# Performance work log

Measured on AMD Instinct MI355X. Metric: run time of the kernel, lower is better.

Reference implementation:

```python
import jax
jax.config.update("jax_enable_x64", True)
import jax.numpy as jnp
import numpy as np

B = 1_000_000

def _generators():
    # 8 sl(3) basis elements, each scaled by its (unit) weight, float64.
    e = np.zeros((8, 3, 3), dtype=np.float64)
    e[0, 0, 2] = 1.0                      # x translation
    e[1, 1, 2] = 1.0                      # y translation
    e[2, 0, 1] = -1.0; e[2, 1, 0] = 1.0   # rotation
    e[3, 0, 0] = 1.0; e[3, 1, 1] = 1.0; e[3, 2, 2] = -2.0  # scale
    e[4, 0, 0] = 1.0; e[4, 1, 1] = -1.0   # stretch
    e[5, 0, 1] = 1.0; e[5, 1, 0] = 1.0    # shear
    e[6, 2, 0] = 1.0                      # x keystone
    e[7, 2, 1] = 1.0                      # y keystone
    weights = np.ones((8,), dtype=np.float64)  # all weight kwargs default to 1.0
    return jnp.asarray(e * weights[:, None, None])

_GEN = _generators()

def setup_inputs() -> dict:
    key = jax.random.key(0)
    lie_vectors = jax.random.normal(key, (B, 8), dtype=jnp.float32)
    return {"lie_vectors": lie_vectors}

def reference(lie_vectors) -> jnp.ndarray:
    # Weighted sum of generators in float64: (B,8) x (8,3,3) -> (B,3,3)
    A = jnp.einsum("bk,kij->bij", lie_vectors.astype(jnp.float64), _GEN)
    # Batched matrix exponential of tiny 3x3 matrices
    H = jax.vmap(jax.scipy.linalg.expm)(A)
    # Homogeneous normalization by the (2,2) entry
    H = H / H[:, 2:3, 2:3]
    return H.astype(jnp.float32)
```

## Files before the change

kernel.cpp:

```cpp
#include <hip/hip_runtime.h>
#include <math.h>

#define BLOCK 256

#define QSTEP(a0, a1, a2, bn)                         \
    {                                                 \
        double n0 = fma(q, a1, bn);                   \
        double n1 = fma(p, a1, q * (a2));             \
        double n2 = fma(p, a2, a0);                   \
        a0 = n0; a1 = n1; a2 = n2;                    \
    }

__global__ __launch_bounds__(BLOCK) void lie_expm_kernel(const float* __restrict__ v,
                                                         float* __restrict__ out,
                                                         int n) {
    __shared__ float lds[BLOCK * 9];

    int tid = threadIdx.x;
    int gid = blockIdx.x * BLOCK + tid;
    bool active = gid < n;

    float oloc[9];

    if (active) {
        const float4* vv = reinterpret_cast<const float4*>(v);
        float4 p0 = vv[2 * (size_t)gid + 0];
        float4 p1 = vv[2 * (size_t)gid + 1];
        double x0 = p0.x, x1 = p0.y, x2 = p0.z, x3 = p0.w;
        double x4 = p1.x, x5 = p1.y, x6 = p1.z, x7 = p1.w;

        double A[9];
        A[0] = x3 + x4;  A[1] = x5 - x2;  A[2] = x0;
        A[3] = x2 + x5;  A[4] = x3 - x4;  A[5] = x1;
        A[6] = x6;       A[7] = x7;       A[8] = -2.0 * x3;

        double c0 = fabs(A[0]) + fabs(A[3]) + fabs(A[6]);
        double c1 = fabs(A[1]) + fabs(A[4]) + fabs(A[7]);
        double c2 = fabs(A[2]) + fabs(A[5]) + fabs(A[8]);
        double nrm = fmax(c0, fmax(c1, c2));

        const double theta13 = 5.371920351148152;
        double r = nrm * (1.0 / theta13);
        int s = 0;
        if (r > 1.0) {
            int hi = __double2hiint(r);
            s = ((hi >> 20) & 0x7ff) - 1023 + 1;
        }
        double sc = __hiloint2double((1023 - s) << 20, 0);
#pragma unroll
        for (int i = 0; i < 9; ++i) A[i] *= sc;

        double A2[9];
#pragma unroll
        for (int i = 0; i < 3; ++i) {
#pragma unroll
            for (int j = 0; j < 3; ++j) {
                A2[i * 3 + j] = fma(A[i * 3 + 0], A[0 * 3 + j],
                                fma(A[i * 3 + 1], A[1 * 3 + j],
                                    A[i * 3 + 2] * A[2 * 3 + j]));
            }
        }

        double p = 0.5 * (A2[0] + A2[4] + A2[8]);
        double q = fma(A[0], fma(A[4], A[8], -A[5] * A[7]),
                   fma(-A[1], fma(A[3], A[8], -A[5] * A[6]),
                       A[2] * fma(A[3], A[7], -A[4] * A[6])));

        const double b0  = 64764752532480000.0, b1  = 32382376266240000.0;
        const double b2  = 7771770303897600.0,  b3  = 1187353796428800.0;
        const double b4  = 129060195264000.0,   b5  = 10559470521600.0;
        const double b6  = 670442572800.0,      b7  = 33522128640.0;
        const double b8  = 1323241920.0,        b9  = 40840800.0;
        const double b10 = 960960.0,            b11 = 16380.0;
        const double b12 = 182.0,               b13 = 1.0;

        double u0 = b13, u1 = 0.0, u2 = 0.0;
        QSTEP(u0, u1, u2, b11)
        QSTEP(u0, u1, u2, b9)
        QSTEP(u0, u1, u2, b7)
        QSTEP(u0, u1, u2, b5)
        QSTEP(u0, u1, u2, b3)
        QSTEP(u0, u1, u2, b1)

        double t0 = b12, t1 = 0.0, t2 = 0.0;
        QSTEP(t0, t1, t2, b10)
        QSTEP(t0, t1, t2, b8)
        QSTEP(t0, t1, t2, b6)
        QSTEP(t0, t1, t2, b4)
        QSTEP(t0, t1, t2, b2)
        QSTEP(t0, t1, t2, b0)

        double U0 = q * u2;
        double U1 = fma(p, u2, u0);
        double U2 = u1;

        double m0 = t0 - U0, m1 = t1 - U1, m2 = t2 - U2;
        double r0 = t0 + U0, r1 = t1 + U1, r2 = t2 + U2;

        double L00 = m0,              L01 = q * m2,          L02 = q * m1;
        double L10 = m1,              L11 = fma(p, m2, m0),  L12 = fma(p, m1, q * m2);
        double L20 = m2,              L21 = m1,              L22 = L11;

        double C00 = fma(L11, L22, -L12 * L21);
        double C01 = fma(L02, L21, -L01 * L22);
        double C02 = fma(L01, L12, -L02 * L11);
        double C10 = fma(L12, L20, -L10 * L22);
        double C11 = fma(L00, L22, -L02 * L20);
        double C12 = fma(L02, L10, -L00 * L12);
        double C20 = fma(L10, L21, -L11 * L20);
        double C21 = fma(L01, L20, -L00 * L21);
        double C22 = fma(L00, L11, -L01 * L10);

        double e0 = fma(C00, r0, fma(C01, r1, C02 * r2));
        double e1 = fma(C10, r0, fma(C11, r1, C12 * r2));
        double e2 = fma(C20, r0, fma(C21, r1, C22 * r2));

        if (s >= 3) {
            double det = fma(L00, C00, fma(L01, C10, L02 * C20));
            double rd = 1.0 / det;
            e0 *= rd; e1 *= rd; e2 *= rd;
        }

        for (int i = 0; i < s; ++i) {
            double d0 = e0 * e0;
            double d1 = 2.0 * e0 * e1;
            double d2 = fma(e1, e1, 2.0 * e0 * e2);
            double d3 = 2.0 * e1 * e2;
            double d4 = e2 * e2;
            e0 = fma(q, d3, d0);
            e1 = fma(p, d3, fma(q, d4, d1));
            e2 = fma(p, d4, d2);
        }

        double H[9];
#pragma unroll
        for (int i = 0; i < 9; ++i) H[i] = fma(e1, A[i], e2 * A2[i]);
        H[0] += e0; H[4] += e0; H[8] += e0;

        double invh = 1.0 / H[8];
#pragma unroll
        for (int i = 0; i < 9; ++i) oloc[i] = (float)(H[i] * invh);
    }

    if (active) {
#pragma unroll
        for (int j = 0; j < 9; ++j) lds[tid * 9 + j] = oloc[j];
    }
    __syncthreads();

    size_t base = (size_t)blockIdx.x * (BLOCK * 9);
    int count = n - blockIdx.x * BLOCK;
    if (count > BLOCK) count = BLOCK;
    int total = count * 9;
#pragma unroll
    for (int i = 0; i < 9; ++i) {
        int idx = i * BLOCK + tid;
        if (idx < total) out[base + idx] = lds[idx];
    }
}

extern "C" void kernel_launch(void* const* d_in, const int* in_sizes, int n_in,
                              void* d_out, int out_size, void* d_ws, size_t ws_size,
                              hipStream_t stream) {
    const float* v = (const float*)d_in[0];
    float* out = (float*)d_out;
    int n = in_sizes[0] / 8;
    int grid = (n + BLOCK - 1) / BLOCK;
    lie_expm_kernel<<<grid, BLOCK, 0, stream>>>(v, out, n);
}
```

Measured before the change: 82.08 us.

## Fold scaling into invariants, use float norm, rcp-Newton, and float4 stores

The scaling exponent is now computed from a single-precision norm, and the 2^-s scaling moves onto the characteristic-polynomial invariants (p·2^-2s, q·2^-3s) and the final coefficients instead of scaling every entry of A. The Padé denominator cofactors are rewritten in terms of a few shared products, the (2,2) entry is fixed to 1, and the double division becomes a hardware reciprocal refined by two Newton steps. Output is written from LDS with float4 stores, and launch bounds request 4 blocks per CU. The aim is to cut FP64 instruction count and store transactions, at the risk of small differences when the float norm lands near a power-of-two boundary.

```diff
diff --git a/kernel.cpp b/kernel.cpp
--- a/kernel.cpp
+++ b/kernel.cpp
@@ -5,50 +5,48 @@
 
 #define QSTEP(a0, a1, a2, bn)                         \
     {                                                 \
-        double n0 = fma(q, a1, bn);                   \
-        double n1 = fma(p, a1, q * (a2));             \
-        double n2 = fma(p, a2, a0);                   \
+        double n0 = fma(qq, a1, bn);                  \
+        double n1 = fma(pp, a1, qq * (a2));           \
+        double n2 = fma(pp, a2, a0);                  \
         a0 = n0; a1 = n1; a2 = n2;                    \
     }
 
-__global__ __launch_bounds__(BLOCK) void lie_expm_kernel(const float* __restrict__ v,
-                                                         float* __restrict__ out,
-                                                         int n) {
+__global__ __launch_bounds__(BLOCK, 4) void lie_expm_kernel(const float* __restrict__ v,
+                                                            float* __restrict__ out,
+                                                            int n) {
     __shared__ float lds[BLOCK * 9];
 
     int tid = threadIdx.x;
     int gid = blockIdx.x * BLOCK + tid;
     bool active = gid < n;
 
-    float oloc[9];
-
     if (active) {
         const float4* vv = reinterpret_cast<const float4*>(v);
         float4 p0 = vv[2 * (size_t)gid + 0];
         float4 p1 = vv[2 * (size_t)gid + 1];
+
+        float c0f = fabsf(p0.w + p1.x) + fabsf(p0.z + p1.y) + fabsf(p1.z);
+        float c1f = fabsf(p1.y - p0.z) + fabsf(p0.w - p1.x) + fabsf(p1.w);
+        float c2f = fabsf(p0.x) + fabsf(p0.y) + 2.0f * fabsf(p0.w);
+        float nrmf = fmaxf(c0f, fmaxf(c1f, c2f));
+        const float inv_theta13 = (float)(1.0 / 5.371920351148152);
+        float rf = nrmf * inv_theta13;
+        int s = 0;
+        if (rf > 1.0f) {
+            int hi = __float_as_int(rf);
+            s = ((hi >> 23) & 0xff) - 127 + 1;
+            if (s > 60) s = 60;
+        }
+        double sc1 = __hiloint2double((1023 - s)     << 20, 0);
+        double sc2 = __hiloint2double((1023 - 2 * s) << 20, 0);
+        double sc3 = __hiloint2double((1023 - 3 * s) << 20, 0);
+
         double x0 = p0.x, x1 = p0.y, x2 = p0.z, x3 = p0.w;
         double x4 = p1.x, x5 = p1.y, x6 = p1.z, x7 = p1.w;
-
         double A[9];
         A[0] = x3 + x4;  A[1] = x5 - x2;  A[2] = x0;
         A[3] = x2 + x5;  A[4] = x3 - x4;  A[5] = x1;
         A[6] = x6;       A[7] = x7;       A[8] = -2.0 * x3;
-
-        double c0 = fabs(A[0]) + fabs(A[3]) + fabs(A[6]);
-        double c1 = fabs(A[1]) + fabs(A[4]) + fabs(A[7]);
-        double c2 = fabs(A[2]) + fabs(A[5]) + fabs(A[8]);
-        double nrm = fmax(c0, fmax(c1, c2));
-
-        const double theta13 = 5.371920351148152;
-        double r = nrm * (1.0 / theta13);
-        int s = 0;
-        if (r > 1.0) {
-            int hi = __double2hiint(r);
-            s = ((hi >> 20) & 0x7ff) - 1023 + 1;
-        }
-        double sc = __hiloint2double((1023 - s) << 20, 0);
-#pragma unroll
-        for (int i = 0; i < 9; ++i) A[i] *= sc;
 
         double A2[9];
 #pragma unroll
@@ -61,10 +59,12 @@
             }
         }
 
-        double p = 0.5 * (A2[0] + A2[4] + A2[8]);
-        double q = fma(A[0], fma(A[4], A[8], -A[5] * A[7]),
-                   fma(-A[1], fma(A[3], A[8], -A[5] * A[6]),
-                       A[2] * fma(A[3], A[7], -A[4] * A[6])));
+        double pu = 0.5 * (A2[0] + A2[4] + A2[8]);
+        double qu = fma(A[0], fma(A[4], A[8], -A[5] * A[7]),
+                    fma(-A[1], fma(A[3], A[8], -A[5] * A[6]),
+                        A[2] * fma(A[3], A[7], -A[4] * A[6])));
+        double pp = pu * sc2;
+        double qq = qu * sc3;
 
         const double b0  = 64764752532480000.0, b1  = 32382376266240000.0;
         const double b2  = 7771770303897600.0,  b3  = 1187353796428800.0;
@@ -90,33 +90,35 @@
         QSTEP(t0, t1, t2, b2)
         QSTEP(t0, t1, t2, b0)
 
-        double U0 = q * u2;
-        double U1 = fma(p, u2, u0);
+        double U0 = qq * u2;
+        double U1 = fma(pp, u2, u0);
         double U2 = u1;
 
-        double m0 = t0 - U0, m1 = t1 - U1, m2 = t2 - U2;
+        double a  = t0 - U0, bq = t1 - U1, c  = t2 - U2;
         double r0 = t0 + U0, r1 = t1 + U1, r2 = t2 + U2;
 
-        double L00 = m0,              L01 = q * m2,          L02 = q * m1;
-        double L10 = m1,              L11 = fma(p, m2, m0),  L12 = fma(p, m1, q * m2);
-        double L20 = m2,              L21 = m1,              L22 = L11;
+        double qc = qq * c;
+        double qb = qq * bq;
+        double d  = fma(pp, c, a);
+        double Le = fma(pp, bq, qc);
+        double ad = a * d;
+        double fb = qb * bq;
+        double c00 = fma(d, d, -Le * bq);
+        double c01 = fb - qc * d;
+        double c02 = fma(qc, Le, -qb * d);
+        double c10 = fma(Le, c, -bq * d);
+        double c11 = fma(-qb, c, ad);
+        double c12 = fb - a * Le;
+        double c20 = fma(bq, bq, -d * c);
+        double c21 = fma(qc, c, -a * bq);
+        double c22 = fma(-qc, bq, ad);
 
-        double C00 = fma(L11, L22, -L12 * L21);
-        double C01 = fma(L02, L21, -L01 * L22);
-        double C02 = fma(L01, L12, -L02 * L11);
-        double C10 = fma(L12, L20, -L10 * L22);
-        double C11 = fma(L00, L22, -L02 * L20);
-        double C12 = fma(L02, L10, -L00 * L12);
-        double C20 = fma(L10, L21, -L11 * L20);
-        double C21 = fma(L01, L20, -L00 * L21);
-        double C22 = fma(L00, L11, -L01 * L10);
-
-        double e0 = fma(C00, r0, fma(C01, r1, C02 * r2));
-        double e1 = fma(C10, r0, fma(C11, r1, C12 * r2));
-        double e2 = fma(C20, r0, fma(C21, r1, C22 * r2));
+        double e0 = fma(c00, r0, fma(c01, r1, c02 * r2));
+        double e1 = fma(c10, r0, fma(c11, r1, c12 * r2));
+        double e2 = fma(c20, r0, fma(c21, r1, c22 * r2));
 
         if (s >= 3) {
-            double det = fma(L00, C00, fma(L01, C10, L02 * C20));
+            double det = fma(a, c00, fma(qc, c10, qb * c20));
             double rd = 1.0 / det;
             e0 *= rd; e1 *= rd; e2 *= rd;
         }
@@ -127,24 +129,29 @@
             double d2 = fma(e1, e1, 2.0 * e0 * e2);
             double d3 = 2.0 * e1 * e2;
             double d4 = e2 * e2;
-            e0 = fma(q, d3, d0);
-            e1 = fma(p, d3, fma(q, d4, d1));
-            e2 = fma(p, d4, d2);
+            e0 = fma(qq, d3, d0);
+            e1 = fma(pp, d3, fma(qq, d4, d1));
+            e2 = fma(pp, d4, d2);
         }
 
-        double H[9];
+        double e1s = e1 * sc1;
+        double e2s = e2 * sc2;
+
+        double H8 = fma(e1s, A[8], fma(e2s, A2[8], e0));
+#if __has_builtin(__builtin_amdgcn_rcp)
+        double invh = __builtin_amdgcn_rcp(H8);
+        invh = fma(invh, fma(-H8, invh, 1.0), invh);
+        invh = fma(invh, fma(-H8, invh, 1.0), invh);
+#else
+        double invh = 1.0 / H8;
+#endif
+
 #pragma unroll
-        for (int i = 0; i < 9; ++i) H[i] = fma(e1, A[i], e2 * A2[i]);
-        H[0] += e0; H[4] += e0; H[8] += e0;
-
-        double invh = 1.0 / H[8];
-#pragma unroll
-        for (int i = 0; i < 9; ++i) oloc[i] = (float)(H[i] * invh);
-    }
-
-    if (active) {
-#pragma unroll
-        for (int j = 0; j < 9; ++j) lds[tid * 9 + j] = oloc[j];
+        for (int i = 0; i < 8; ++i) {
+            double Hi = fma(e1s, A[i], fma(e2s, A2[i], (i == 0 || i == 4) ? e0 : 0.0));
+            lds[tid * 9 + i] = (float)(Hi * invh);
+        }
+        lds[tid * 9 + 8] = 1.0f;
     }
     __syncthreads();
 
@@ -152,11 +159,17 @@
     int count = n - blockIdx.x * BLOCK;
     if (count > BLOCK) count = BLOCK;
     int total = count * 9;
+    int nf4 = total >> 2;
+    float4* out4 = reinterpret_cast<float4*>(out + base);
+    const float4* lds4 = reinterpret_cast<const float4*>(lds);
 #pragma unroll
-    for (int i = 0; i < 9; ++i) {
+    for (int i = 0; i < 3; ++i) {
         int idx = i * BLOCK + tid;
-        if (idx < total) out[base + idx] = lds[idx];
+        if (idx < nf4) out4[idx] = lds4[idx];
     }
+    int remstart = nf4 << 2;
+    int ridx = remstart + tid;
+    if (ridx < total) out[base + ridx] = lds[ridx];
 }
 
 extern "C" void kernel_launch(void* const* d_in, const int* in_sizes, int n_in,
```

New measurement: 81.67 us. Within noise of the previous version (-0.5%).
